# Performance work log

Hardware: AMD Instinct MI355X
Metric: run time of the kernel (lower is better)

Reference implementation:

```python
import jax, jax.numpy as jnp
import numpy as np

B, T, D = 4, 8192, 512
E, F, CAP = 8, 2048, 4096


def setup_inputs() -> dict:
    key = jax.random.key(0)
    ks = jax.random.split(key, 6)
    s = 0.02
    return {
        "x": jax.random.normal(ks[0], (B, T, D), dtype=jnp.float32),
        "Wr": jax.random.normal(ks[1], (D, E), dtype=jnp.float32) * s,
        "W1": jax.random.normal(ks[2], (E, D, F), dtype=jnp.float32) * s,
        "b1": jax.random.normal(ks[3], (E, F), dtype=jnp.float32) * s,
        "W2": jax.random.normal(ks[4], (E, F, D), dtype=jnp.float32) * s,
        "b2": jax.random.normal(ks[5], (E, D), dtype=jnp.float32) * s,
    }


def reference(x, Wr, W1, b1, W2, b2):
    Bb, Tt, Dd = x.shape
    N = Bb * Tt
    C = min(CAP, N)
    x_flat = x.reshape(N, Dd)
    logits = x_flat @ Wr                      # [N, E]
    probs = jax.nn.softmax(logits, axis=0)    # softmax over tokens (dim=0)
    # per-expert top-C tokens
    vals, idx = jax.lax.top_k(probs.T, C)     # [E, C]
    selected = x_flat[idx]                    # [E, C, D] gather
    h = jax.nn.gelu(jnp.einsum('ecd,edf->ecf', selected, W1) + b1[:, None, :],
                    approximate=False)
    out_e = jnp.einsum('ecf,efd->ecd', h, W2) + b2[:, None, :]  # [E, C, D]
    weighted = vals[..., None] * out_e
    output = jnp.zeros_like(x_flat).at[idx.reshape(-1)].add(weighted.reshape(-1, Dd))
    return output.reshape(Bb, Tt, Dd)
```

## Files before the change

kernel.cpp:

```cpp
#include <hip/hip_runtime.h>
#include <math.h>

#define N_TOK 32768
#define DIM 512
#define NE 8
#define NF 2048
#define CCAP 4096

typedef __attribute__((ext_vector_type(4))) float floatx4;
typedef __attribute__((ext_vector_type(8))) short shortx8;
typedef __attribute__((ext_vector_type(4))) short shortx4;

__device__ __forceinline__ short f2bf(float f) {
  union { float f; unsigned u; } v; v.f = f;
  unsigned r = v.u + 0x7FFFu + ((v.u >> 16) & 1u);
  return (short)(r >> 16);
}

__device__ __forceinline__ unsigned f2key(float f) {
  union { float f; unsigned u; } v; v.f = f;
  return (v.u & 0x80000000u) ? ~v.u : (v.u | 0x80000000u);
}

__device__ __forceinline__ void gll16(const void* g, void* l) {
  __builtin_amdgcn_global_load_lds(
      (const __attribute__((address_space(1))) void*)g,
      (__attribute__((address_space(3))) void*)l, 16, 0, 0);
}

__device__ __forceinline__ float fast_gelu(float h) {
  float u = 0.7978845608f * (h + 0.044715f * h * h * h);
  float au = fabsf(u) * 2.885390082f;
  float z = __builtin_amdgcn_exp2f(au);
  float th = 1.0f - 2.0f * __builtin_amdgcn_rcpf(1.0f + z);
  th = copysignf(th, u);
  return 0.5f * h * (1.0f + th);
}

__global__ __launch_bounds__(256) void k_prep(
    const float* __restrict__ x, const float* __restrict__ W1,
    const float* __restrict__ W2, const float* __restrict__ Wr,
    float* __restrict__ out, short* __restrict__ xb,
    short* __restrict__ w1t, short* __restrict__ w2t,
    float* __restrict__ logitsT) {
  __shared__ float tl[64 * 68];
  const int b = blockIdx.x, t = threadIdx.x;
  if (b < 4096) {
    const float* in;
    short* o;
    int R, C, c0, r0;
    if (b < 2048) {
      int e = b >> 8, tlid = b & 255;
      in = W1 + (size_t)e * DIM * NF;
      o = w1t + (size_t)e * NF * DIM;
      R = DIM; C = NF;
      c0 = (tlid & 31) * 64; r0 = (tlid >> 5) * 64;
    } else {
      int bb = b - 2048;
      int e = bb >> 8, tlid = bb & 255;
      in = W2 + (size_t)e * NF * DIM;
      o = w2t + (size_t)e * DIM * NF;
      R = NF; C = DIM;
      c0 = (tlid & 7) * 64; r0 = (tlid >> 3) * 64;
    }
    const int r = t >> 4, cq = (t & 15) * 4;
#pragma unroll
    for (int ii = 0; ii < 4; ii++) {
      floatx4 v = *(const floatx4*)&in[(size_t)(r0 + r + 16 * ii) * C + c0 + cq];
      *(floatx4*)&tl[(r + 16 * ii) * 68 + cq] = v;
    }
    __syncthreads();
    const int cc = t >> 2, rq = (t & 3) * 16;
    shortx8 o0, o1;
#pragma unroll
    for (int k = 0; k < 8; k++) o0[k] = f2bf(tl[(rq + k) * 68 + cc]);
#pragma unroll
    for (int k = 0; k < 8; k++) o1[k] = f2bf(tl[(rq + 8 + k) * 68 + cc]);
    size_t ob = (size_t)(c0 + cc) * R + r0 + rq;
    *(shortx8*)&o[ob] = o0;
    *(shortx8*)&o[ob + 8] = o1;
  } else if (b < 4608) {
    const int base = (b - 4096) * 8192 + t;
    floatx4 z = {0.f, 0.f, 0.f, 0.f};
#pragma unroll
    for (int i = 0; i < 32; i++) *(floatx4*)&out[(size_t)(base + i * 256) * 4] = z;
  } else if (b < 5120) {
    const int base = (b - 4608) * 8192 + t;
#pragma unroll
    for (int i = 0; i < 32; i++) {
      floatx4 v = *(const floatx4*)&x[(size_t)(base + i * 256) * 4];
      shortx4 s;
      s.x = f2bf(v.x); s.y = f2bf(v.y); s.z = f2bf(v.z); s.w = f2bf(v.w);
      *(shortx4*)&xb[(size_t)(base + i * 256) * 4] = s;
    }
  } else {
    const int lane = t & 63;
    const int wave = (b - 5120) * 4 + (t >> 6);
    float wr[64];
#pragma unroll
    for (int i = 0; i < 16; i++)
      *(floatx4*)&wr[i * 4] = *(const floatx4*)&Wr[lane * 64 + i * 4];
    for (int n = wave; n < N_TOK; n += 4096) {
      const float* xr = x + (size_t)n * DIM + lane * 8;
      floatx4 x0 = *(const floatx4*)xr;
      floatx4 x1 = *(const floatx4*)(xr + 4);
      float xs[8] = {x0.x, x0.y, x0.z, x0.w, x1.x, x1.y, x1.z, x1.w};
      double acc[8];
#pragma unroll
      for (int e2 = 0; e2 < 8; e2++) acc[e2] = 0.0;
#pragma unroll
      for (int j = 0; j < 8; j++) {
        double xv = (double)xs[j];
#pragma unroll
        for (int e2 = 0; e2 < 8; e2++) acc[e2] += xv * (double)wr[j * 8 + e2];
      }
#pragma unroll
      for (int e2 = 0; e2 < 8; e2++) {
#pragma unroll
        for (int off2 = 32; off2 > 0; off2 >>= 1)
          acc[e2] += __shfl_xor(acc[e2], off2);
      }
      double rv = acc[0];
#pragma unroll
      for (int e2 = 1; e2 < 8; e2++)
        if (lane == e2) rv = acc[e2];
      if (lane < 8) logitsT[(size_t)lane * N_TOK + n] = (float)rv;
    }
  }
}

__global__ __launch_bounds__(1024) void k_select(const float* __restrict__ logitsT,
                                                 int* __restrict__ sel_idx,
                                                 float* __restrict__ sel_val) {
  __shared__ float redf[16];
  __shared__ unsigned redu[16];
  __shared__ float s_max, s_inv;
  __shared__ unsigned s_tot;
  __shared__ unsigned s_cnt[2];
  const int e = blockIdx.x, t = threadIdx.x;
  const int wid = t >> 6, lane = t & 63;
  const float* lg = logitsT + (size_t)e * N_TOK;
  float lv[32];
  unsigned kv[32];
#pragma unroll
  for (int i = 0; i < 32; i++) lv[i] = lg[i * 1024 + t];
#pragma unroll
  for (int i = 0; i < 32; i++) kv[i] = f2key(lv[i]);
  float m = lv[0];
#pragma unroll
  for (int i = 1; i < 32; i++) m = fmaxf(m, lv[i]);
#pragma unroll
  for (int o = 32; o > 0; o >>= 1) m = fmaxf(m, __shfl_xor(m, o));
  if (lane == 0) redf[wid] = m;
  __syncthreads();
  if (t == 0) {
    float v = redf[0];
    for (int i = 1; i < 16; i++) v = fmaxf(v, redf[i]);
    s_max = v;
  }
  __syncthreads();
  m = s_max;
  float s = 0.f;
#pragma unroll
  for (int i = 0; i < 32; i++) s += expf(lv[i] - m);
#pragma unroll
  for (int o = 32; o > 0; o >>= 1) s += __shfl_xor(s, o);
  if (lane == 0) redf[wid] = s;
  __syncthreads();
  if (t == 0) {
    float v = 0.f;
    for (int i = 0; i < 16; i++) v += redf[i];
    s_inv = 1.0f / v;
  }
  unsigned T = 0;
  for (int bb = 31; bb >= 0; --bb) {
    unsigned cand = T | (1u << bb);
    unsigned c = 0;
#pragma unroll
    for (int i = 0; i < 32; i++) c += (kv[i] >= cand) ? 1u : 0u;
#pragma unroll
    for (int o = 32; o > 0; o >>= 1) c += __shfl_xor(c, o);
    if (lane == 0) redu[wid] = c;
    __syncthreads();
    if (t == 0) {
      unsigned v = 0;
      for (int i = 0; i < 16; i++) v += redu[i];
      s_tot = v;
    }
    __syncthreads();
    if (s_tot >= CCAP) T = cand;
  }
  {
    unsigned c = 0;
#pragma unroll
    for (int i = 0; i < 32; i++) c += (kv[i] > T) ? 1u : 0u;
#pragma unroll
    for (int o = 32; o > 0; o >>= 1) c += __shfl_xor(c, o);
    if (lane == 0) redu[wid] = c;
    __syncthreads();
    if (t == 0) {
      unsigned v = 0;
      for (int i = 0; i < 16; i++) v += redu[i];
      s_tot = v;
      s_cnt[0] = 0;
      s_cnt[1] = 0;
    }
    __syncthreads();
  }
  const unsigned rr = CCAP - s_tot;
  const float inv = s_inv;
  const unsigned long long lmask = (1ull << lane) - 1ull;
#pragma unroll
  for (int i = 0; i < 32; i++) {
    int n = i * 1024 + t;
    bool gt = kv[i] > T;
    bool eq = kv[i] == T;
    unsigned long long mg = __ballot(gt);
    unsigned long long mq = __ballot(eq);
    unsigned bg = 0, bq = 0;
    if (lane == 0) {
      if (mg) bg = atomicAdd(&s_cnt[0], (unsigned)__popcll(mg));
      if (mq) bq = atomicAdd(&s_cnt[1], (unsigned)__popcll(mq));
    }
    bg = __shfl(bg, 0);
    bq = __shfl(bq, 0);
    int pos = -1;
    if (gt) {
      pos = (int)(bg + (unsigned)__popcll(mg & lmask));
    } else if (eq) {
      unsigned qq = bq + (unsigned)__popcll(mq & lmask);
      if (qq < rr) pos = (int)(CCAP - rr + qq);
    }
    if (pos >= 0) {
      sel_idx[e * CCAP + pos] = n;
      sel_val[e * CCAP + pos] = expf(lv[i] - m) * inv;
    }
  }
}

__global__ __launch_bounds__(256, 2) void k_gemm1(
    const short* __restrict__ xb, const short* __restrict__ w1t,
    const float* __restrict__ b1, const int* __restrict__ sel_idx,
    short* __restrict__ H, int e0) {
  __shared__ char smem[256 * 136 * 2];
  short* ldsA = (short*)smem;
  const int zi = blockIdx.z;
  const int e = e0 + zi;
  const int c0 = blockIdx.y * 256;
  const int f0 = blockIdx.x * 128;
  const int t = threadIdx.x;
  const int lane = t & 63;
  const int w = t >> 6;
  const int wm = w & 1, wn = w >> 1;
  const int row8 = t >> 3;
  const int su = (t & 7) ^ (row8 & 7);

  const short* gAp[8];
#pragma unroll
  for (int i = 0; i < 8; i++) {
    int tok = sel_idx[e * CCAP + c0 + row8 + i * 32];
    gAp[i] = xb + (size_t)tok * DIM + su * 8;
  }
  const short* gB = w1t + ((size_t)(e * NF + f0 + wn * 64 + (lane & 15))) * DIM + (lane >> 4) * 8;

  floatx4 acc[8][4];
#pragma unroll
  for (int i = 0; i < 8; i++)
#pragma unroll
    for (int j = 0; j < 4; j++) acc[i][j] = (floatx4){0.f, 0.f, 0.f, 0.f};

  const int arow = wm * 128 + (lane & 15);
  const int lx = lane & 7, q = lane >> 4;

  for (int kk = 0; kk < DIM / 64; ++kk) {
    __syncthreads();
#pragma unroll
    for (int i = 0; i < 8; i++) gll16(gAp[i], ldsA + i * 2048 + t * 8);
#pragma unroll
    for (int i = 0; i < 8; i++) gAp[i] += 64;
    __syncthreads();
#pragma unroll
    for (int g = 0; g < 2; g++) {
      const int pu = ((((g << 2) | q)) ^ lx) << 3;
      shortx8 bf[4];
#pragma unroll
      for (int j = 0; j < 4; j++)
        bf[j] = *(const shortx8*)(gB + (size_t)j * 16 * DIM + kk * 64 + g * 32);
      shortx8 af[8];
#pragma unroll
      for (int i = 0; i < 8; i++)
        af[i] = *(const shortx8*)&ldsA[(arow + i * 16) * 64 + pu];
#pragma unroll
      for (int i = 0; i < 8; i++)
#pragma unroll
        for (int j = 0; j < 4; j++)
          acc[i][j] = __builtin_amdgcn_mfma_f32_16x16x32_bf16(af[i], bf[j], acc[i][j], 0, 0, 0);
    }
  }

  __syncthreads();
  short* ep = (short*)smem;
  const int colL = wn * 64 + (lane & 15);
  const int rowL = wm * 128 + ((lane >> 4) << 2);
#pragma unroll
  for (int j = 0; j < 4; j++) {
    float bv = b1[e * NF + f0 + colL + j * 16];
#pragma unroll
    for (int i = 0; i < 8; i++) {
#pragma unroll
      for (int r = 0; r < 4; r++) {
        float h = acc[i][j][r] + bv;
        ep[(rowL + i * 16 + r) * 136 + colL + j * 16] = f2bf(fast_gelu(h));
      }
    }
  }
  __syncthreads();
  short* Hp = H + (size_t)zi * CCAP * NF;
  const int chunk = t & 15;
#pragma unroll
  for (int it = 0; it < 16; it++) {
    int r = (t >> 4) + 16 * it;
    shortx8 v = *(const shortx8*)&ep[r * 136 + chunk * 8];
    *(shortx8*)&Hp[(size_t)(c0 + r) * NF + f0 + chunk * 8] = v;
  }
}

__global__ __launch_bounds__(256, 2) void k_gemm2(
    const short* __restrict__ H, const short* __restrict__ w2t,
    const float* __restrict__ b2, const int* __restrict__ sel_idx,
    const float* __restrict__ sel_val, float* __restrict__ out, int e0) {
  __shared__ short ldsA[256 * 64];
  __shared__ int tokL[256];
  __shared__ float valL[256];
  const int zi = blockIdx.z;
  const int e = e0 + zi;
  const int c0 = blockIdx.y * 256;
  const int d0 = blockIdx.x * 128;
  const int t = threadIdx.x;
  const int lane = t & 63;
  const int w = t >> 6;
  const int wm = w & 1, wn = w >> 1;
  tokL[t] = sel_idx[e * CCAP + c0 + t];
  valL[t] = sel_val[e * CCAP + c0 + t];
  const int row8 = t >> 3;
  const int su = (t & 7) ^ (row8 & 7);

  const short* gA = H + ((size_t)zi * CCAP + c0 + row8) * NF + su * 8;
  const short* gB = w2t + ((size_t)(e * DIM + d0 + wn * 64 + (lane & 15))) * NF + (lane >> 4) * 8;

  floatx4 acc[8][4];
#pragma unroll
  for (int i = 0; i < 8; i++)
#pragma unroll
    for (int j = 0; j < 4; j++) acc[i][j] = (floatx4){0.f, 0.f, 0.f, 0.f};

  const int arow = wm * 128 + (lane & 15);
  const int lx = lane & 7, q = lane >> 4;

  for (int kk = 0; kk < NF / 64; ++kk) {
    __syncthreads();
#pragma unroll
    for (int i = 0; i < 8; i++)
      gll16(gA + (size_t)i * 32 * NF + kk * 64, ldsA + i * 2048 + t * 8);
    __syncthreads();
#pragma unroll
    for (int g = 0; g < 2; g++) {
      const int pu = ((((g << 2) | q)) ^ lx) << 3;
      shortx8 bf[4];
#pragma unroll
      for (int j = 0; j < 4; j++)
        bf[j] = *(const shortx8*)(gB + (size_t)j * 16 * NF + kk * 64 + g * 32);
      shortx8 af[8];
#pragma unroll
      for (int i = 0; i < 8; i++)
        af[i] = *(const shortx8*)&ldsA[(arow + i * 16) * 64 + pu];
#pragma unroll
      for (int i = 0; i < 8; i++)
#pragma unroll
        for (int j = 0; j < 4; j++)
          acc[i][j] = __builtin_amdgcn_mfma_f32_16x16x32_bf16(af[i], bf[j], acc[i][j], 0, 0, 0);
    }
  }

  const int colL = wn * 64 + (lane & 15);
  const int rowL = wm * 128 + ((lane >> 4) << 2);
#pragma unroll
  for (int j = 0; j < 4; j++) {
    float bv = b2[e * DIM + d0 + colL + j * 16];
#pragma unroll
    for (int i = 0; i < 8; i++) {
#pragma unroll
      for (int r = 0; r < 4; r++) {
        int row = rowL + i * 16 + r;
        float o = acc[i][j][r] + bv;
        atomicAdd(&out[(size_t)tokL[row] * DIM + d0 + colL + j * 16], valL[row] * o);
      }
    }
  }
}

extern "C" void kernel_launch(void* const* d_in, const int* in_sizes, int n_in,
                              void* d_out, int out_size, void* d_ws, size_t ws_size,
                              hipStream_t stream) {
  const float* x = (const float*)d_in[0];
  const float* Wr = (const float*)d_in[1];
  const float* W1 = (const float*)d_in[2];
  const float* b1 = (const float*)d_in[3];
  const float* W2 = (const float*)d_in[4];
  const float* b2 = (const float*)d_in[5];
  float* out = (float*)d_out;

  char* p = (char*)d_ws;
  size_t off = 0;
  auto carve = [&](size_t bytes) {
    void* r = p + off;
    off = (off + bytes + 255) & ~(size_t)255;
    return r;
  };
  short* xb = (short*)carve((size_t)N_TOK * DIM * 2);
  short* w1t = (short*)carve((size_t)NE * NF * DIM * 2);
  short* w2t = (short*)carve((size_t)NE * DIM * NF * 2);
  float* logitsT = (float*)carve((size_t)NE * N_TOK * 4);
  int* selidx = (int*)carve((size_t)NE * CCAP * 4);
  float* selval = (float*)carve((size_t)NE * CCAP * 4);
  const size_t hbytes = (size_t)CCAP * NF * 2;
  int g = 1;
  if (off + 8 * hbytes <= ws_size) g = 8;
  else if (off + 4 * hbytes <= ws_size) g = 4;
  else if (off + 2 * hbytes <= ws_size) g = 2;
  short* Hbuf = (short*)carve((size_t)g * hbytes);

  k_prep<<<6144, 256, 0, stream>>>(x, W1, W2, Wr, out, xb, w1t, w2t, logitsT);
  k_select<<<NE, 1024, 0, stream>>>(logitsT, selidx, selval);
  for (int e0 = 0; e0 < NE; e0 += g) {
    k_gemm1<<<dim3(NF / 128, CCAP / 256, g), 256, 0, stream>>>(xb, w1t, b1, selidx, Hbuf, e0);
    k_gemm2<<<dim3(DIM / 128, CCAP / 256, g), 256, 0, stream>>>(Hbuf, w2t, b2, selidx, selval, out, e0);
  }
}
```

Before: 588.3 us.

## Double-buffer LDS A tiles and remap block order so experts interleave

Both expert GEMM kernels now stage the gathered A tile into two LDS buffers, so the next 64-wide K slice is loaded while the current one feeds the MFMAs. This removes one barrier per iteration and hides global-to-LDS latency. Block IDs are also remapped so consecutive blocks cover different experts, which spreads the atomic traffic in gemm2 and the weight reads across experts. The cost is 64KB of LDS in gemm2, which may lower occupancy below the two blocks per CU set in launch bounds.

```diff
diff --git a/kernel.cpp b/kernel.cpp
--- a/kernel.cpp
+++ b/kernel.cpp
@@ -35,6 +35,41 @@
   float th = 1.0f - 2.0f * __builtin_amdgcn_rcpf(1.0f + z);
   th = copysignf(th, u);
   return 0.5f * h * (1.0f + th);
+}
+
+__device__ __forceinline__ void stage8_adv(const short** ap, short* dst, int t) {
+#pragma unroll
+  for (int i = 0; i < 8; i++) gll16(ap[i], dst + i * 2048 + t * 8);
+#pragma unroll
+  for (int i = 0; i < 8; i++) ap[i] += 64;
+}
+
+__device__ __forceinline__ void stage8_g2(const short* gA, short* dst, int t, int kk) {
+#pragma unroll
+  for (int i = 0; i < 8; i++)
+    gll16(gA + (size_t)i * 32 * NF + kk * 64, dst + i * 2048 + t * 8);
+}
+
+__device__ __forceinline__ void compute64(const short* ldsA, const short* gB,
+                                          floatx4 (*acc)[4], int arow, int lx, int q,
+                                          int koff, int ldb) {
+#pragma unroll
+  for (int g = 0; g < 2; g++) {
+    const int pu = (((g << 2) | q) ^ lx) << 3;
+    shortx8 bf[4];
+#pragma unroll
+    for (int j = 0; j < 4; j++)
+      bf[j] = *(const shortx8*)(gB + (size_t)j * 16 * ldb + koff + g * 32);
+    shortx8 af[8];
+#pragma unroll
+    for (int i = 0; i < 8; i++)
+      af[i] = *(const shortx8*)&ldsA[(arow + i * 16) * 64 + pu];
+#pragma unroll
+    for (int i = 0; i < 8; i++)
+#pragma unroll
+      for (int j = 0; j < 4; j++)
+        acc[i][j] = __builtin_amdgcn_mfma_f32_16x16x32_bf16(af[i], bf[j], acc[i][j], 0, 0, 0);
+  }
 }
 
 __global__ __launch_bounds__(256) void k_prep(
@@ -243,11 +278,22 @@
     const float* __restrict__ b1, const int* __restrict__ sel_idx,
     short* __restrict__ H, int e0) {
   __shared__ char smem[256 * 136 * 2];
-  short* ldsA = (short*)smem;
-  const int zi = blockIdx.z;
+  short* ldsA0 = (short*)smem;
+  short* ldsA1 = (short*)(smem + 32768);
+
+  int bx, by, zi;
+  if (gridDim.z == 8) {
+    int lid = blockIdx.x + (blockIdx.y << 4) + (blockIdx.z << 8);
+    zi = lid & 7;
+    int rem = lid >> 3;
+    bx = rem & 15;
+    by = rem >> 4;
+  } else {
+    bx = blockIdx.x; by = blockIdx.y; zi = blockIdx.z;
+  }
   const int e = e0 + zi;
-  const int c0 = blockIdx.y * 256;
-  const int f0 = blockIdx.x * 128;
+  const int c0 = by * 256;
+  const int f0 = bx * 128;
   const int t = threadIdx.x;
   const int lane = t & 63;
   const int w = t >> 6;
@@ -272,33 +318,17 @@
   const int arow = wm * 128 + (lane & 15);
   const int lx = lane & 7, q = lane >> 4;
 
-  for (int kk = 0; kk < DIM / 64; ++kk) {
-    __syncthreads();
-#pragma unroll
-    for (int i = 0; i < 8; i++) gll16(gAp[i], ldsA + i * 2048 + t * 8);
-#pragma unroll
-    for (int i = 0; i < 8; i++) gAp[i] += 64;
-    __syncthreads();
-#pragma unroll
-    for (int g = 0; g < 2; g++) {
-      const int pu = ((((g << 2) | q)) ^ lx) << 3;
-      shortx8 bf[4];
-#pragma unroll
-      for (int j = 0; j < 4; j++)
-        bf[j] = *(const shortx8*)(gB + (size_t)j * 16 * DIM + kk * 64 + g * 32);
-      shortx8 af[8];
-#pragma unroll
-      for (int i = 0; i < 8; i++)
-        af[i] = *(const shortx8*)&ldsA[(arow + i * 16) * 64 + pu];
-#pragma unroll
-      for (int i = 0; i < 8; i++)
-#pragma unroll
-        for (int j = 0; j < 4; j++)
-          acc[i][j] = __builtin_amdgcn_mfma_f32_16x16x32_bf16(af[i], bf[j], acc[i][j], 0, 0, 0);
-    }
-  }
-
-  __syncthreads();
+  stage8_adv(gAp, ldsA0, t);
+  __syncthreads();
+  for (int kk = 0; kk < DIM / 64; kk += 2) {
+    stage8_adv(gAp, ldsA1, t);
+    compute64(ldsA0, gB, acc, arow, lx, q, kk * 64, DIM);
+    __syncthreads();
+    if (kk + 2 < DIM / 64) stage8_adv(gAp, ldsA0, t);
+    compute64(ldsA1, gB, acc, arow, lx, q, (kk + 1) * 64, DIM);
+    __syncthreads();
+  }
+
   short* ep = (short*)smem;
   const int colL = wn * 64 + (lane & 15);
   const int rowL = wm * 128 + ((lane >> 4) << 2);
@@ -329,13 +359,25 @@
     const short* __restrict__ H, const short* __restrict__ w2t,
     const float* __restrict__ b2, const int* __restrict__ sel_idx,
     const float* __restrict__ sel_val, float* __restrict__ out, int e0) {
-  __shared__ short ldsA[256 * 64];
-  __shared__ int tokL[256];
-  __shared__ float valL[256];
-  const int zi = blockIdx.z;
+  __shared__ char smem[2 * 32768 + 256 * 4 + 256 * 4];
+  short* ldsA0 = (short*)smem;
+  short* ldsA1 = (short*)(smem + 32768);
+  int* tokL = (int*)(smem + 65536);
+  float* valL = (float*)(smem + 65536 + 1024);
+
+  int bx, by, zi;
+  if (gridDim.z == 8) {
+    int lid = blockIdx.x + (blockIdx.y << 2) + (blockIdx.z << 6);
+    zi = lid & 7;
+    int rem = lid >> 3;
+    bx = rem & 3;
+    by = rem >> 2;
+  } else {
+    bx = blockIdx.x; by = blockIdx.y; zi = blockIdx.z;
+  }
   const int e = e0 + zi;
-  const int c0 = blockIdx.y * 256;
-  const int d0 = blockIdx.x * 128;
+  const int c0 = by * 256;
+  const int d0 = bx * 128;
   const int t = threadIdx.x;
   const int lane = t & 63;
   const int w = t >> 6;
@@ -357,29 +399,15 @@
   const int arow = wm * 128 + (lane & 15);
   const int lx = lane & 7, q = lane >> 4;
 
-  for (int kk = 0; kk < NF / 64; ++kk) {
-    __syncthreads();
-#pragma unroll
-    for (int i = 0; i < 8; i++)
-      gll16(gA + (size_t)i * 32 * NF + kk * 64, ldsA + i * 2048 + t * 8);
-    __syncthreads();
-#pragma unroll
-    for (int g = 0; g < 2; g++) {
-      const int pu = ((((g << 2) | q)) ^ lx) << 3;
-      shortx8 bf[4];
-#pragma unroll
-      for (int j = 0; j < 4; j++)
-        bf[j] = *(const shortx8*)(gB + (size_t)j * 16 * NF + kk * 64 + g * 32);
-      shortx8 af[8];
-#pragma unroll
-      for (int i = 0; i < 8; i++)
-        af[i] = *(const shortx8*)&ldsA[(arow + i * 16) * 64 + pu];
-#pragma unroll
-      for (int i = 0; i < 8; i++)
-#pragma unroll
-        for (int j = 0; j < 4; j++)
-          acc[i][j] = __builtin_amdgcn_mfma_f32_16x16x32_bf16(af[i], bf[j], acc[i][j], 0, 0, 0);
-    }
+  stage8_g2(gA, ldsA0, t, 0);
+  __syncthreads();
+  for (int kk = 0; kk < NF / 64; kk += 2) {
+    stage8_g2(gA, ldsA1, t, kk + 1);
+    compute64(ldsA0, gB, acc, arow, lx, q, kk * 64, NF);
+    __syncthreads();
+    if (kk + 2 < NF / 64) stage8_g2(gA, ldsA0, t, kk + 2);
+    compute64(ldsA1, gB, acc, arow, lx, q, (kk + 1) * 64, NF);
+    __syncthreads();
   }
 
   const int colL = wn * 64 + (lane & 15);
```

Result: faster. 557.9 us (-5.2%).
